# Kernel optimization log

Measured on AMD Instinct MI355X. Metric: run time of the kernel, lower is better.

Reference implementation:

```python
import jax, jax.numpy as jnp
import numpy as np

EPS = 1e-12  # matches torch F.normalize default eps


def _l2norm(x):
    n = jnp.linalg.norm(x, axis=-1, keepdims=True)
    return x / jnp.maximum(n, EPS)


def setup_inputs() -> dict:
    key = jax.random.key(0)
    k1, k2, k3, k4 = jax.random.split(key, 4)
    B, N, Lq, Ld, D = 64, 16, 32, 256, 128
    query_rep = jax.random.normal(k1, (B, Lq, D), jnp.float32)
    doc_reps = jax.random.normal(k2, (B, N, Ld, D), jnp.float32)
    doc_mask = jax.random.randint(k3, (B, N, Ld), 0, 2).astype(jnp.int32)
    labels = jax.random.normal(k4, (B, 2 * N), jnp.float32)
    return {"query_rep": query_rep, "doc_reps": doc_reps,
            "doc_mask": doc_mask, "labels": labels}


def reference(query_rep, doc_reps, doc_mask, labels):
    # ColBERT MaxSim: normalize query tokens (no mask, as in original),
    # mask+normalize doc tokens, bmm, max over doc tokens, sum over query tokens.
    q = _l2norm(query_rep)                                   # [B,Lq,D]
    d = _l2norm(doc_reps * doc_mask[..., None].astype(doc_reps.dtype))  # [B,N,Ld,D]
    tok = jnp.einsum('bqd,bnld->bnql', q, d)                 # [B,N,Lq,Ld]
    scores = tok.max(axis=-1).sum(axis=-1)                   # [B,N]

    # Pairwise ranking loss
    N = scores.shape[1]
    ys = labels[:, :N]
    idx = labels[:, N:]
    diffs = jnp.triu(scores[:, :, None] - scores[:, None, :])    # [B,N,N], lower tri zeroed
    weights = jnp.abs(idx[:, :, None] - idx[:, None, :])
    pairs = (ys[:, :, None] - ys[:, None, :]) > 0
    losses = jnp.log1p(jnp.exp(-diffs)) * weights
    return jnp.sum(jnp.where(pairs, losses, 0.0))
```

## Files before the change

kernel.cpp:

```cpp
#include <hip/hip_runtime.h>
#include <cmath>

#define EPSN 1e-12f

typedef _Float16 half8 __attribute__((ext_vector_type(8)));
typedef float f32x4 __attribute__((ext_vector_type(4)));

__global__ __launch_bounds__(256, 4) void scores_kernel(
    const float* __restrict__ qr, const float* __restrict__ doc,
    const int* __restrict__ mask, float* __restrict__ pmax) {
    __shared__ __align__(16) char Aimg[16384];
    __shared__ __align__(16) char Bimg[16384];
    __shared__ float ssPart[256];
    __shared__ float invS[128];
    __shared__ float wq[4][32];

    int t = threadIdx.x, g = blockIdx.x;
    int bn = g >> 1, h = g & 1, b = g >> 5;
    int w = t >> 6, lane = t & 63, col = lane & 15;
    int tok = t & 127, kh = t >> 7;

    int row = t >> 3, jb = t & 7;
    const float4* qsrc = (const float4*)(qr + ((size_t)b * 32 + row) * 128 + jb * 16);
    float4 v0 = qsrc[0], v1 = qsrc[1], v2 = qsrc[2], v3 = qsrc[3];

    const float4* dsrc = (const float4*)(doc + ((size_t)bn * 256 + h * 128 + tok) * 128) + kh * 4;
    float4 rA0 = dsrc[0],  rA1 = dsrc[1],  rA2 = dsrc[2],  rA3 = dsrc[3];
    float4 rB0 = dsrc[8],  rB1 = dsrc[9],  rB2 = dsrc[10], rB3 = dsrc[11];
    float4 rC0, rC1, rC2, rC3;
    int mymask = 0;
    if (t < 128) mymask = mask[bn * 256 + h * 128 + t];

    {
        float ss = v0.x*v0.x + v0.y*v0.y + v0.z*v0.z + v0.w*v0.w
                 + v1.x*v1.x + v1.y*v1.y + v1.z*v1.z + v1.w*v1.w
                 + v2.x*v2.x + v2.y*v2.y + v2.z*v2.z + v2.w*v2.w
                 + v3.x*v3.x + v3.y*v3.y + v3.z*v3.z + v3.w*v3.w;
        ss += __shfl_xor(ss, 1); ss += __shfl_xor(ss, 2); ss += __shfl_xor(ss, 4);
        float inv = 1.0f / fmaxf(sqrtf(ss), EPSN);
        int qt = row >> 4, kstep = jb >> 1;
        float4 vv[4] = { v0, v1, v2, v3 };
#pragma unroll
        for (int khh = 0; khh < 2; ++khh) {
            float xs[8] = { vv[2*khh].x,   vv[2*khh].y,   vv[2*khh].z,   vv[2*khh].w,
                            vv[2*khh+1].x, vv[2*khh+1].y, vv[2*khh+1].z, vv[2*khh+1].w };
            half8 hh, hl;
#pragma unroll
            for (int e = 0; e < 8; ++e) {
                float x = xs[e] * inv;
                _Float16 hv = (_Float16)x;
                hh[e] = hv;
                hl[e] = (_Float16)(x - (float)hv);
            }
            int quad = (jb & 1) * 2 + khh;
            int base = ((qt * 4 + kstep) * 2) * 1024 + ((row & 15) + quad * 16) * 16;
            *(half8*)(Aimg + base)        = hh;
            *(half8*)(Aimg + base + 1024) = hl;
        }
    }
    asm volatile("s_waitcnt lgkmcnt(0)" ::: "memory");
    __builtin_amdgcn_s_barrier();

    f32x4 acc[2][2];
    f32x4 zero = {0.f, 0.f, 0.f, 0.f};
    acc[0][0] = zero; acc[0][1] = zero; acc[1][0] = zero; acc[1][1] = zero;
    float ss_d = 0.f;

    int tile8 = tok >> 4;
    int bo_base = tile8 * 2048 + (2 * kh) * 256 + (tok & 15) * 16;

#define CHUNK(C, P0, P1, P2, P3, N0, N1, N2, N3, PREF, ISLAST) do {           \
    if (PREF) {                                                               \
        N0 = dsrc[(C + 2) * 8 + 0]; N1 = dsrc[(C + 2) * 8 + 1];               \
        N2 = dsrc[(C + 2) * 8 + 2]; N3 = dsrc[(C + 2) * 8 + 3];               \
    }                                                                         \
    ss_d += P0.x*P0.x + P0.y*P0.y + P0.z*P0.z + P0.w*P0.w;                    \
    ss_d += P1.x*P1.x + P1.y*P1.y + P1.z*P1.z + P1.w*P1.w;                    \
    ss_d += P2.x*P2.x + P2.y*P2.y + P2.z*P2.z + P2.w*P2.w;                    \
    ss_d += P3.x*P3.x + P3.y*P3.y + P3.z*P3.z + P3.w*P3.w;                    \
    {                                                                         \
        float xa[8] = { P0.x, P0.y, P0.z, P0.w, P1.x, P1.y, P1.z, P1.w };     \
        float xb[8] = { P2.x, P2.y, P2.z, P2.w, P3.x, P3.y, P3.z, P3.w };     \
        half8 hha, hla, hhb, hlb;                                             \
        _Pragma("unroll")                                                     \
        for (int e = 0; e < 8; ++e) {                                         \
            float x = xa[e]; _Float16 hv = (_Float16)x;                       \
            hha[e] = hv; hla[e] = (_Float16)(x - (float)hv);                  \
            float y = xb[e]; _Float16 hw = (_Float16)y;                       \
            hhb[e] = hw; hlb[e] = (_Float16)(y - (float)hw);                  \
        }                                                                     \
        *(half8*)(Bimg + bo_base)              = hha;                         \
        *(half8*)(Bimg + bo_base + 1024)       = hla;                         \
        *(half8*)(Bimg + bo_base + 256)        = hhb;                         \
        *(half8*)(Bimg + bo_base + 256 + 1024) = hlb;                         \
    }                                                                         \
    if (ISLAST) ssPart[t] = ss_d;                                             \
    asm volatile("s_waitcnt lgkmcnt(0)" ::: "memory");                        \
    __builtin_amdgcn_s_barrier();                                             \
    if ((ISLAST) && t < 128) {                                                \
        float sst = ssPart[t] + ssPart[t + 128];                              \
        invS[t] = mymask ? (1.0f / fmaxf(sqrtf(sst), EPSN)) : 0.0f;           \
    }                                                                         \
    {                                                                         \
        int lo = lane << 4;                                                   \
        half8 a0h = *(const half8*)(Aimg + (((C) * 2 + 0) << 10) + lo);       \
        half8 a0l = *(const half8*)(Aimg + (((C) * 2 + 1) << 10) + lo);       \
        half8 a1h = *(const half8*)(Aimg + (((4 + (C)) * 2 + 0) << 10) + lo); \
        half8 a1l = *(const half8*)(Aimg + (((4 + (C)) * 2 + 1) << 10) + lo); \
        _Pragma("unroll")                                                     \
        for (int nt = 0; nt < 2; ++nt) {                                      \
            int tile = w * 2 + nt;                                            \
            half8 bh = *(const half8*)(Bimg + tile * 2048 + lo);              \
            half8 bl = *(const half8*)(Bimg + tile * 2048 + 1024 + lo);       \
            acc[0][nt] = __builtin_amdgcn_mfma_f32_16x16x32_f16(a0l, bh, acc[0][nt], 0, 0, 0); \
            acc[0][nt] = __builtin_amdgcn_mfma_f32_16x16x32_f16(a0h, bl, acc[0][nt], 0, 0, 0); \
            acc[0][nt] = __builtin_amdgcn_mfma_f32_16x16x32_f16(a0h, bh, acc[0][nt], 0, 0, 0); \
            acc[1][nt] = __builtin_amdgcn_mfma_f32_16x16x32_f16(a1l, bh, acc[1][nt], 0, 0, 0); \
            acc[1][nt] = __builtin_amdgcn_mfma_f32_16x16x32_f16(a1h, bl, acc[1][nt], 0, 0, 0); \
            acc[1][nt] = __builtin_amdgcn_mfma_f32_16x16x32_f16(a1h, bh, acc[1][nt], 0, 0, 0); \
        }                                                                     \
    }                                                                         \
    asm volatile("s_waitcnt lgkmcnt(0)" ::: "memory");                        \
    __builtin_amdgcn_s_barrier();                                             \
} while (0)

    CHUNK(0, rA0, rA1, rA2, rA3, rC0, rC1, rC2, rC3, 1, false);
    CHUNK(1, rB0, rB1, rB2, rB3, rA0, rA1, rA2, rA3, 1, false);
    CHUNK(2, rC0, rC1, rC2, rC3, rB0, rB1, rB2, rB3, 0, false);
    CHUNK(3, rA0, rA1, rA2, rA3, rB0, rB1, rB2, rB3, 0, true);
#undef CHUNK

    float inv0 = invS[w * 32 + col];
    float inv1 = invS[w * 32 + 16 + col];
    float m8[8];
#pragma unroll
    for (int qt = 0; qt < 2; ++qt)
#pragma unroll
        for (int rr = 0; rr < 4; ++rr)
            m8[qt * 4 + rr] = fmaxf(acc[qt][0][rr] * inv0, acc[qt][1][rr] * inv1);
#pragma unroll
    for (int off = 1; off < 16; off <<= 1)
#pragma unroll
        for (int i = 0; i < 8; ++i) m8[i] = fmaxf(m8[i], __shfl_xor(m8[i], off));
    if (col == 0) {
        int rg = lane >> 4;
#pragma unroll
        for (int qt = 0; qt < 2; ++qt)
#pragma unroll
            for (int rr = 0; rr < 4; ++rr) wq[w][qt * 16 + rg * 4 + rr] = m8[qt * 4 + rr];
    }
    __syncthreads();
    if (w == 0 && lane < 32) {
        float v = fmaxf(fmaxf(wq[0][lane], wq[1][lane]), fmaxf(wq[2][lane], wq[3][lane]));
        pmax[(size_t)g * 32 + lane] = v;
    }
}

__global__ __launch_bounds__(256) void lossb_kernel(const float* __restrict__ pmax,
                                                    const float* __restrict__ labels,
                                                    float* __restrict__ partial) {
    __shared__ float pmL[1024];
    __shared__ float sc[16], ysS[16], idxS[16];
    __shared__ float wsum[4];
    int b = blockIdx.x, t = threadIdx.x;
    ((float4*)pmL)[t] = ((const float4*)(pmax + (size_t)b * 1024))[t];
    if (t < 16) { ysS[t] = labels[b * 32 + t]; idxS[t] = labels[b * 32 + 16 + t]; }
    __syncthreads();
    {
        int n = t >> 4, qq = t & 15;
        float v = fmaxf(pmL[n * 64 + qq],      pmL[n * 64 + 32 + qq])
                + fmaxf(pmL[n * 64 + 16 + qq], pmL[n * 64 + 48 + qq]);
        v += __shfl_xor(v, 1); v += __shfl_xor(v, 2);
        v += __shfl_xor(v, 4); v += __shfl_xor(v, 8);
        if (qq == 0) sc[n] = v;
    }
    __syncthreads();
    int i = t >> 4, j = t & 15;
    float v = 0.f;
    if (ysS[i] - ysS[j] > 0.f) {
        float wgt = fabsf(idxS[i] - idxS[j]);
        float d = (i <= j) ? (sc[i] - sc[j]) : 0.f;
        v = log1pf(expf(-d)) * wgt;
    }
#pragma unroll
    for (int off = 1; off < 64; off <<= 1) v += __shfl_xor(v, off);
    int lane = t & 63;
    if (lane == 0) wsum[t >> 6] = v;
    __syncthreads();
    if (t == 0) partial[b] = wsum[0] + wsum[1] + wsum[2] + wsum[3];
}

__global__ void lossfin_kernel(const float* __restrict__ partial, float* __restrict__ out) {
    int t = threadIdx.x;
    float v = partial[t];
#pragma unroll
    for (int off = 1; off < 64; off <<= 1) v += __shfl_xor(v, off);
    if (t == 0) out[0] = v;
}

extern "C" void kernel_launch(void* const* d_in, const int* in_sizes, int n_in,
                              void* d_out, int out_size, void* d_ws, size_t ws_size,
                              hipStream_t stream) {
    const float* qr     = (const float*)d_in[0];
    const float* doc    = (const float*)d_in[1];
    const int*   dmask  = (const int*)d_in[2];
    const float* labels = (const float*)d_in[3];
    float* out = (float*)d_out;

    float* pmax    = (float*)d_ws;
    float* partial = pmax + 2048 * 32;

    scores_kernel<<<2048, 256, 0, stream>>>(qr, doc, dmask, pmax);
    lossb_kernel<<<64, 256, 0, stream>>>(pmax, labels, partial);
    lossfin_kernel<<<1, 64, 0, stream>>>(partial, out);
}
```

Baseline: 34.63 us.

## Compact unmasked doc tokens and skip loading and converting masked ones

Each block now ballots the doc mask, builds a compacted list of unmasked token indices in shared memory, and maps threads to compacted slots. Only real tokens are loaded from global memory, squared-summed and split into fp16 hi/lo. Unused B tile slots are zeroed once and get an inverse norm of 0, so the max still sees the zero scores that masked tokens produce in the reference. This is meant to cut global memory traffic and conversion work roughly in proportion to the masked fraction, at the cost of two extra block syncs and divergent loads.

```diff
diff --git a/kernel.cpp b/kernel.cpp
--- a/kernel.cpp
+++ b/kernel.cpp
@@ -13,23 +13,41 @@
     __shared__ __align__(16) char Bimg[16384];
     __shared__ float ssPart[256];
     __shared__ float invS[128];
+    __shared__ int   compactS[128];
+    __shared__ int   cntW[2];
     __shared__ float wq[4][32];
 
     int t = threadIdx.x, g = blockIdx.x;
     int bn = g >> 1, h = g & 1, b = g >> 5;
     int w = t >> 6, lane = t & 63, col = lane & 15;
-    int tok = t & 127, kh = t >> 7;
 
     int row = t >> 3, jb = t & 7;
     const float4* qsrc = (const float4*)(qr + ((size_t)b * 32 + row) * 128 + jb * 16);
     float4 v0 = qsrc[0], v1 = qsrc[1], v2 = qsrc[2], v3 = qsrc[3];
 
-    const float4* dsrc = (const float4*)(doc + ((size_t)bn * 256 + h * 128 + tok) * 128) + kh * 4;
-    float4 rA0 = dsrc[0],  rA1 = dsrc[1],  rA2 = dsrc[2],  rA3 = dsrc[3];
-    float4 rB0 = dsrc[8],  rB1 = dsrc[9],  rB2 = dsrc[10], rB3 = dsrc[11];
-    float4 rC0, rC1, rC2, rC3;
-    int mymask = 0;
-    if (t < 128) mymask = mask[bn * 256 + h * 128 + t];
+    int myMask = 0;
+    if (t < 128) myMask = mask[bn * 256 + h * 128 + t];
+    unsigned long long bal = __ballot(myMask != 0);
+    if (t < 128 && lane == 0) cntW[w] = __popcll(bal);
+    __syncthreads();
+    int cnt = cntW[0] + cntW[1];
+    if (myMask) {
+        int prefix = __popcll(bal & ((1ull << lane) - 1));
+        int basec = (w == 1) ? cntW[0] : 0;
+        compactS[basec + prefix] = t;
+    }
+    __syncthreads();
+
+    int s = t & 127, kh = t >> 7;
+    bool real = (s < cnt);
+    int tokc = real ? compactS[s] : 0;
+
+    const float4* dsrc = (const float4*)(doc + ((size_t)bn * 256 + h * 128 + tokc) * 128) + kh * 4;
+    float4 rA0, rA1, rA2, rA3, rB0, rB1, rB2, rB3, rC0, rC1, rC2, rC3;
+    if (real) {
+        rA0 = dsrc[0];  rA1 = dsrc[1];  rA2 = dsrc[2],  rA3 = dsrc[3];
+        rB0 = dsrc[8];  rB1 = dsrc[9];  rB2 = dsrc[10]; rB3 = dsrc[11];
+    }
 
     {
         float ss = v0.x*v0.x + v0.y*v0.y + v0.z*v0.z + v0.w*v0.w
@@ -66,19 +84,19 @@
     acc[0][0] = zero; acc[0][1] = zero; acc[1][0] = zero; acc[1][1] = zero;
     float ss_d = 0.f;
 
-    int tile8 = tok >> 4;
-    int bo_base = tile8 * 2048 + (2 * kh) * 256 + (tok & 15) * 16;
+    int tile8 = s >> 4;
+    int bo_base = tile8 * 2048 + (2 * kh) * 256 + (s & 15) * 16;
 
 #define CHUNK(C, P0, P1, P2, P3, N0, N1, N2, N3, PREF, ISLAST) do {           \
-    if (PREF) {                                                               \
+    if ((PREF) && real) {                                                     \
         N0 = dsrc[(C + 2) * 8 + 0]; N1 = dsrc[(C + 2) * 8 + 1];               \
         N2 = dsrc[(C + 2) * 8 + 2]; N3 = dsrc[(C + 2) * 8 + 3];               \
     }                                                                         \
-    ss_d += P0.x*P0.x + P0.y*P0.y + P0.z*P0.z + P0.w*P0.w;                    \
-    ss_d += P1.x*P1.x + P1.y*P1.y + P1.z*P1.z + P1.w*P1.w;                    \
-    ss_d += P2.x*P2.x + P2.y*P2.y + P2.z*P2.z + P2.w*P2.w;                    \
-    ss_d += P3.x*P3.x + P3.y*P3.y + P3.z*P3.z + P3.w*P3.w;                    \
-    {                                                                         \
+    if (real) {                                                               \
+        ss_d += P0.x*P0.x + P0.y*P0.y + P0.z*P0.z + P0.w*P0.w;                \
+        ss_d += P1.x*P1.x + P1.y*P1.y + P1.z*P1.z + P1.w*P1.w;                \
+        ss_d += P2.x*P2.x + P2.y*P2.y + P2.z*P2.z + P2.w*P2.w;                \
+        ss_d += P3.x*P3.x + P3.y*P3.y + P3.z*P3.z + P3.w*P3.w;                \
         float xa[8] = { P0.x, P0.y, P0.z, P0.w, P1.x, P1.y, P1.z, P1.w };     \
         float xb[8] = { P2.x, P2.y, P2.z, P2.w, P3.x, P3.y, P3.z, P3.w };     \
         half8 hha, hla, hhb, hlb;                                             \
@@ -93,13 +111,19 @@
         *(half8*)(Bimg + bo_base + 1024)       = hla;                         \
         *(half8*)(Bimg + bo_base + 256)        = hhb;                         \
         *(half8*)(Bimg + bo_base + 256 + 1024) = hlb;                         \
+    } else if ((C) == 0) {                                                    \
+        half8 hz = {0,0,0,0,0,0,0,0};                                         \
+        *(half8*)(Bimg + bo_base)              = hz;                          \
+        *(half8*)(Bimg + bo_base + 1024)       = hz;                          \
+        *(half8*)(Bimg + bo_base + 256)        = hz;                          \
+        *(half8*)(Bimg + bo_base + 256 + 1024) = hz;                          \
     }                                                                         \
     if (ISLAST) ssPart[t] = ss_d;                                             \
     asm volatile("s_waitcnt lgkmcnt(0)" ::: "memory");                        \
     __builtin_amdgcn_s_barrier();                                             \
     if ((ISLAST) && t < 128) {                                                \
         float sst = ssPart[t] + ssPart[t + 128];                              \
-        invS[t] = mymask ? (1.0f / fmaxf(sqrtf(sst), EPSN)) : 0.0f;           \
+        invS[t] = (t < cnt) ? (1.0f / fmaxf(sqrtf(sst), EPSN)) : 0.0f;        \
     }                                                                         \
     {                                                                         \
         int lo = lane << 4;                                                   \
```

New measurement: 30.03 us (median of 2 runs). -13.3%, faster.

## Compact unmasked doc tokens and skip loading masked rows

Applied to the files above, without the earlier changes.

Each block now handles 64 doc tokens instead of 128. A wave ballot over the mask builds a compacted list of unmasked tokens, and only those rows are loaded from global memory; the remaining slots are zero-filled with a zero inverse norm. This removes HBM traffic for masked tokens, which contribute only zero to the max anyway. In exchange the grid doubles, the chunked prefetch pipeline is replaced by a single load phase, the LDS tile grows, and the loss kernel reduces four partial maxima per query instead of two.

```diff
diff --git a/kernel.cpp b/kernel.cpp
--- a/kernel.cpp
+++ b/kernel.cpp
@@ -6,30 +6,44 @@
 typedef _Float16 half8 __attribute__((ext_vector_type(8)));
 typedef float f32x4 __attribute__((ext_vector_type(4)));
 
-__global__ __launch_bounds__(256, 4) void scores_kernel(
+__global__ __launch_bounds__(256, 3) void scores_kernel(
     const float* __restrict__ qr, const float* __restrict__ doc,
     const int* __restrict__ mask, float* __restrict__ pmax) {
     __shared__ __align__(16) char Aimg[16384];
-    __shared__ __align__(16) char Bimg[16384];
-    __shared__ float ssPart[256];
-    __shared__ float invS[128];
+    __shared__ __align__(16) char Bimg[32768];
+    __shared__ float invS[64];
+    __shared__ int   compactS[64];
+    __shared__ int   cntS;
     __shared__ float wq[4][32];
 
     int t = threadIdx.x, g = blockIdx.x;
-    int bn = g >> 1, h = g & 1, b = g >> 5;
+    int bn = g >> 2, q4 = g & 3, b = g >> 6;
     int w = t >> 6, lane = t & 63, col = lane & 15;
-    int tok = t & 127, kh = t >> 7;
 
     int row = t >> 3, jb = t & 7;
     const float4* qsrc = (const float4*)(qr + ((size_t)b * 32 + row) * 128 + jb * 16);
     float4 v0 = qsrc[0], v1 = qsrc[1], v2 = qsrc[2], v3 = qsrc[3];
 
-    const float4* dsrc = (const float4*)(doc + ((size_t)bn * 256 + h * 128 + tok) * 128) + kh * 4;
-    float4 rA0 = dsrc[0],  rA1 = dsrc[1],  rA2 = dsrc[2],  rA3 = dsrc[3];
-    float4 rB0 = dsrc[8],  rB1 = dsrc[9],  rB2 = dsrc[10], rB3 = dsrc[11];
-    float4 rC0, rC1, rC2, rC3;
-    int mymask = 0;
-    if (t < 128) mymask = mask[bn * 256 + h * 128 + t];
+    int myMask = 0;
+    if (t < 64) myMask = mask[bn * 256 + q4 * 64 + t];
+    unsigned long long bal = __ballot(myMask != 0);
+    if (t == 0) cntS = __popcll(bal);
+    if (myMask) {
+        int prefix = __popcll(bal & ((1ull << lane) - 1));
+        compactS[prefix] = t;
+    }
+    __syncthreads();
+    int cnt = cntS;
+    int s = t >> 2, kq = t & 3;
+    bool real = (s < cnt);
+    int tokc = real ? compactS[s] : 0;
+
+    const float4* dsrc = (const float4*)(doc + ((size_t)bn * 256 + q4 * 64 + tokc) * 128) + kq * 8;
+    float4 r0, r1, r2, r3, r4, r5, r6, r7;
+    if (real) {
+        r0 = dsrc[0]; r1 = dsrc[1]; r2 = dsrc[2]; r3 = dsrc[3];
+        r4 = dsrc[4]; r5 = dsrc[5]; r6 = dsrc[6]; r7 = dsrc[7];
+    }
 
     {
         float ss = v0.x*v0.x + v0.y*v0.y + v0.z*v0.z + v0.w*v0.w
@@ -58,86 +72,72 @@
             *(half8*)(Aimg + base + 1024) = hl;
         }
     }
+
+    int tileS = s >> 4, colS = s & 15;
+    int bo0 = tileS * 8192 + kq * 2048 + colS * 16;
+    float ss_d = 0.f;
+    if (real) {
+        ss_d = r0.x*r0.x + r0.y*r0.y + r0.z*r0.z + r0.w*r0.w
+             + r1.x*r1.x + r1.y*r1.y + r1.z*r1.z + r1.w*r1.w
+             + r2.x*r2.x + r2.y*r2.y + r2.z*r2.z + r2.w*r2.w
+             + r3.x*r3.x + r3.y*r3.y + r3.z*r3.z + r3.w*r3.w
+             + r4.x*r4.x + r4.y*r4.y + r4.z*r4.z + r4.w*r4.w
+             + r5.x*r5.x + r5.y*r5.y + r5.z*r5.z + r5.w*r5.w
+             + r6.x*r6.x + r6.y*r6.y + r6.z*r6.z + r6.w*r6.w
+             + r7.x*r7.x + r7.y*r7.y + r7.z*r7.z + r7.w*r7.w;
+#define CVTQ(PA, PB, QD) do {                                                 \
+        float xs[8] = { PA.x, PA.y, PA.z, PA.w, PB.x, PB.y, PB.z, PB.w };     \
+        half8 hh, hl;                                                         \
+        _Pragma("unroll")                                                     \
+        for (int e = 0; e < 8; ++e) {                                         \
+            float x = xs[e]; _Float16 hv = (_Float16)x;                       \
+            hh[e] = hv; hl[e] = (_Float16)(x - (float)hv);                    \
+        }                                                                     \
+        *(half8*)(Bimg + bo0 + (QD) * 256)        = hh;                       \
+        *(half8*)(Bimg + bo0 + (QD) * 256 + 1024) = hl;                       \
+    } while (0)
+        CVTQ(r0, r1, 0); CVTQ(r2, r3, 1); CVTQ(r4, r5, 2); CVTQ(r6, r7, 3);
+#undef CVTQ
+    } else {
+        half8 hz = {0,0,0,0,0,0,0,0};
+#pragma unroll
+        for (int qd = 0; qd < 4; ++qd) {
+            *(half8*)(Bimg + bo0 + qd * 256)        = hz;
+            *(half8*)(Bimg + bo0 + qd * 256 + 1024) = hz;
+        }
+    }
+    ss_d += __shfl_xor(ss_d, 1); ss_d += __shfl_xor(ss_d, 2);
+    if (kq == 0) invS[s] = real ? (1.0f / fmaxf(sqrtf(ss_d), EPSN)) : 0.0f;
+
     asm volatile("s_waitcnt lgkmcnt(0)" ::: "memory");
     __builtin_amdgcn_s_barrier();
 
-    f32x4 acc[2][2];
-    f32x4 zero = {0.f, 0.f, 0.f, 0.f};
-    acc[0][0] = zero; acc[0][1] = zero; acc[1][0] = zero; acc[1][1] = zero;
-    float ss_d = 0.f;
-
-    int tile8 = tok >> 4;
-    int bo_base = tile8 * 2048 + (2 * kh) * 256 + (tok & 15) * 16;
-
-#define CHUNK(C, P0, P1, P2, P3, N0, N1, N2, N3, PREF, ISLAST) do {           \
-    if (PREF) {                                                               \
-        N0 = dsrc[(C + 2) * 8 + 0]; N1 = dsrc[(C + 2) * 8 + 1];               \
-        N2 = dsrc[(C + 2) * 8 + 2]; N3 = dsrc[(C + 2) * 8 + 3];               \
-    }                                                                         \
-    ss_d += P0.x*P0.x + P0.y*P0.y + P0.z*P0.z + P0.w*P0.w;                    \
-    ss_d += P1.x*P1.x + P1.y*P1.y + P1.z*P1.z + P1.w*P1.w;                    \
-    ss_d += P2.x*P2.x + P2.y*P2.y + P2.z*P2.z + P2.w*P2.w;                    \
-    ss_d += P3.x*P3.x + P3.y*P3.y + P3.z*P3.z + P3.w*P3.w;                    \
-    {                                                                         \
-        float xa[8] = { P0.x, P0.y, P0.z, P0.w, P1.x, P1.y, P1.z, P1.w };     \
-        float xb[8] = { P2.x, P2.y, P2.z, P2.w, P3.x, P3.y, P3.z, P3.w };     \
-        half8 hha, hla, hhb, hlb;                                             \
-        _Pragma("unroll")                                                     \
-        for (int e = 0; e < 8; ++e) {                                         \
-            float x = xa[e]; _Float16 hv = (_Float16)x;                       \
-            hha[e] = hv; hla[e] = (_Float16)(x - (float)hv);                  \
-            float y = xb[e]; _Float16 hw = (_Float16)y;                       \
-            hhb[e] = hw; hlb[e] = (_Float16)(y - (float)hw);                  \
-        }                                                                     \
-        *(half8*)(Bimg + bo_base)              = hha;                         \
-        *(half8*)(Bimg + bo_base + 1024)       = hla;                         \
-        *(half8*)(Bimg + bo_base + 256)        = hhb;                         \
-        *(half8*)(Bimg + bo_base + 256 + 1024) = hlb;                         \
-    }                                                                         \
-    if (ISLAST) ssPart[t] = ss_d;                                             \
-    asm volatile("s_waitcnt lgkmcnt(0)" ::: "memory");                        \
-    __builtin_amdgcn_s_barrier();                                             \
-    if ((ISLAST) && t < 128) {                                                \
-        float sst = ssPart[t] + ssPart[t + 128];                              \
-        invS[t] = mymask ? (1.0f / fmaxf(sqrtf(sst), EPSN)) : 0.0f;           \
-    }                                                                         \
-    {                                                                         \
-        int lo = lane << 4;                                                   \
-        half8 a0h = *(const half8*)(Aimg + (((C) * 2 + 0) << 10) + lo);       \
-        half8 a0l = *(const half8*)(Aimg + (((C) * 2 + 1) << 10) + lo);       \
-        half8 a1h = *(const half8*)(Aimg + (((4 + (C)) * 2 + 0) << 10) + lo); \
-        half8 a1l = *(const half8*)(Aimg + (((4 + (C)) * 2 + 1) << 10) + lo); \
-        _Pragma("unroll")                                                     \
-        for (int nt = 0; nt < 2; ++nt) {                                      \
-            int tile = w * 2 + nt;                                            \
-            half8 bh = *(const half8*)(Bimg + tile * 2048 + lo);              \
-            half8 bl = *(const half8*)(Bimg + tile * 2048 + 1024 + lo);       \
-            acc[0][nt] = __builtin_amdgcn_mfma_f32_16x16x32_f16(a0l, bh, acc[0][nt], 0, 0, 0); \
-            acc[0][nt] = __builtin_amdgcn_mfma_f32_16x16x32_f16(a0h, bl, acc[0][nt], 0, 0, 0); \
-            acc[0][nt] = __builtin_amdgcn_mfma_f32_16x16x32_f16(a0h, bh, acc[0][nt], 0, 0, 0); \
-            acc[1][nt] = __builtin_amdgcn_mfma_f32_16x16x32_f16(a1l, bh, acc[1][nt], 0, 0, 0); \
-            acc[1][nt] = __builtin_amdgcn_mfma_f32_16x16x32_f16(a1h, bl, acc[1][nt], 0, 0, 0); \
-            acc[1][nt] = __builtin_amdgcn_mfma_f32_16x16x32_f16(a1h, bh, acc[1][nt], 0, 0, 0); \
-        }                                                                     \
-    }                                                                         \
-    asm volatile("s_waitcnt lgkmcnt(0)" ::: "memory");                        \
-    __builtin_amdgcn_s_barrier();                                             \
-} while (0)
-
-    CHUNK(0, rA0, rA1, rA2, rA3, rC0, rC1, rC2, rC3, 1, false);
-    CHUNK(1, rB0, rB1, rB2, rB3, rA0, rA1, rA2, rA3, 1, false);
-    CHUNK(2, rC0, rC1, rC2, rC3, rB0, rB1, rB2, rB3, 0, false);
-    CHUNK(3, rA0, rA1, rA2, rA3, rB0, rB1, rB2, rB3, 0, true);
-#undef CHUNK
-
-    float inv0 = invS[w * 32 + col];
-    float inv1 = invS[w * 32 + 16 + col];
+    f32x4 acc0 = {0.f, 0.f, 0.f, 0.f};
+    f32x4 acc1 = {0.f, 0.f, 0.f, 0.f};
+    int lo = lane << 4;
+#pragma unroll
+    for (int k2 = 0; k2 < 4; ++k2) {
+        half8 a0h = *(const half8*)(Aimg + ((0 * 4 + k2) * 2 + 0) * 1024 + lo);
+        half8 a0l = *(const half8*)(Aimg + ((0 * 4 + k2) * 2 + 1) * 1024 + lo);
+        half8 a1h = *(const half8*)(Aimg + ((1 * 4 + k2) * 2 + 0) * 1024 + lo);
+        half8 a1l = *(const half8*)(Aimg + ((1 * 4 + k2) * 2 + 1) * 1024 + lo);
+        half8 bh  = *(const half8*)(Bimg + w * 8192 + k2 * 2048 + lo);
+        half8 bl  = *(const half8*)(Bimg + w * 8192 + k2 * 2048 + 1024 + lo);
+        acc0 = __builtin_amdgcn_mfma_f32_16x16x32_f16(a0l, bh, acc0, 0, 0, 0);
+        acc0 = __builtin_amdgcn_mfma_f32_16x16x32_f16(a0h, bl, acc0, 0, 0, 0);
+        acc0 = __builtin_amdgcn_mfma_f32_16x16x32_f16(a0h, bh, acc0, 0, 0, 0);
+        acc1 = __builtin_amdgcn_mfma_f32_16x16x32_f16(a1l, bh, acc1, 0, 0, 0);
+        acc1 = __builtin_amdgcn_mfma_f32_16x16x32_f16(a1h, bl, acc1, 0, 0, 0);
+        acc1 = __builtin_amdgcn_mfma_f32_16x16x32_f16(a1h, bh, acc1, 0, 0, 0);
+    }
+
+    float inv = invS[w * 16 + col];
     float m8[8];
 #pragma unroll
-    for (int qt = 0; qt < 2; ++qt)
-#pragma unroll
-        for (int rr = 0; rr < 4; ++rr)
-            m8[qt * 4 + rr] = fmaxf(acc[qt][0][rr] * inv0, acc[qt][1][rr] * inv1);
+    for (int rr = 0; rr < 4; ++rr) {
+        m8[rr]     = acc0[rr] * inv;
+        m8[4 + rr] = acc1[rr] * inv;
+    }
 #pragma unroll
     for (int off = 1; off < 16; off <<= 1)
 #pragma unroll
@@ -145,9 +145,10 @@
     if (col == 0) {
         int rg = lane >> 4;
 #pragma unroll
-        for (int qt = 0; qt < 2; ++qt)
-#pragma unroll
-            for (int rr = 0; rr < 4; ++rr) wq[w][qt * 16 + rg * 4 + rr] = m8[qt * 4 + rr];
+        for (int rr = 0; rr < 4; ++rr) {
+            wq[w][rg * 4 + rr]      = m8[rr];
+            wq[w][16 + rg * 4 + rr] = m8[4 + rr];
+        }
     }
     __syncthreads();
     if (w == 0 && lane < 32) {
@@ -159,17 +160,21 @@
 __global__ __launch_bounds__(256) void lossb_kernel(const float* __restrict__ pmax,
                                                     const float* __restrict__ labels,
                                                     float* __restrict__ partial) {
-    __shared__ float pmL[1024];
+    __shared__ float pmL[2048];
     __shared__ float sc[16], ysS[16], idxS[16];
     __shared__ float wsum[4];
     int b = blockIdx.x, t = threadIdx.x;
-    ((float4*)pmL)[t] = ((const float4*)(pmax + (size_t)b * 1024))[t];
+    ((float4*)pmL)[t]       = ((const float4*)(pmax + (size_t)b * 2048))[t];
+    ((float4*)pmL)[t + 256] = ((const float4*)(pmax + (size_t)b * 2048))[t + 256];
     if (t < 16) { ysS[t] = labels[b * 32 + t]; idxS[t] = labels[b * 32 + 16 + t]; }
     __syncthreads();
     {
         int n = t >> 4, qq = t & 15;
-        float v = fmaxf(pmL[n * 64 + qq],      pmL[n * 64 + 32 + qq])
-                + fmaxf(pmL[n * 64 + 16 + qq], pmL[n * 64 + 48 + qq]);
+        float ma = fmaxf(fmaxf(pmL[(n * 4 + 0) * 32 + qq],      pmL[(n * 4 + 1) * 32 + qq]),
+                         fmaxf(pmL[(n * 4 + 2) * 32 + qq],      pmL[(n * 4 + 3) * 32 + qq]));
+        float mb = fmaxf(fmaxf(pmL[(n * 4 + 0) * 32 + 16 + qq], pmL[(n * 4 + 1) * 32 + 16 + qq]),
+                         fmaxf(pmL[(n * 4 + 2) * 32 + 16 + qq], pmL[(n * 4 + 3) * 32 + 16 + qq]));
+        float v = ma + mb;
         v += __shfl_xor(v, 1); v += __shfl_xor(v, 2);
         v += __shfl_xor(v, 4); v += __shfl_xor(v, 8);
         if (qq == 0) sc[n] = v;
@@ -208,9 +213,9 @@
     float* out = (float*)d_out;
 
     float* pmax    = (float*)d_ws;
-    float* partial = pmax + 2048 * 32;
-
-    scores_kernel<<<2048, 256, 0, stream>>>(qr, doc, dmask, pmax);
+    float* partial = pmax + 4096 * 32;
+
+    scores_kernel<<<4096, 256, 0, stream>>>(qr, doc, dmask, pmax);
     lossb_kernel<<<64, 256, 0, stream>>>(pmax, labels, partial);
     lossfin_kernel<<<1, 64, 0, stream>>>(partial, out);
 }
```

New measurement: 40.97 us. 18.3% more time.
